# Kernel tuning notes

Hardware: AMD Instinct MI355X
Metric: run time of the kernel (lower is better)

The kernel has to match this reference:

```python
import jax, jax.numpy as jnp
import numpy as np
from jax import lax

NUM_TAGS = 9
HIDDEN = 768
BATCH = 64
SEQ = 512


def setup_inputs() -> dict:
    key = jax.random.key(0)
    ks = jax.random.split(key, 6)
    hidden = jax.random.normal(ks[0], (BATCH, SEQ, HIDDEN), dtype=jnp.float32)
    labels = jax.random.randint(ks[1], (BATCH, SEQ), 0, NUM_TAGS)  # all >= 0 -> full mask
    weight = jax.random.normal(ks[2], (NUM_TAGS, HIDDEN), dtype=jnp.float32) * 0.02
    bias = jnp.zeros((NUM_TAGS,), dtype=jnp.float32)
    start_transitions = jax.random.normal(ks[3], (NUM_TAGS,), dtype=jnp.float32) * 0.1
    end_transitions = jax.random.normal(ks[4], (NUM_TAGS,), dtype=jnp.float32) * 0.1
    transitions = jax.random.normal(ks[5], (NUM_TAGS, NUM_TAGS), dtype=jnp.float32) * 0.1
    return dict(hidden=hidden, labels=labels, weight=weight, bias=bias,
                start_transitions=start_transitions, end_transitions=end_transitions,
                transitions=transitions)


def _crf_log_likelihood(emissions, tags, mask, start_t, end_t, trans):
    """pytorch-crf log-likelihood, reduction='sum'.
    emissions [B,L,T] float, tags [B,L] int, mask [B,L] bool."""
    # --- numerator: score of the gold path ---
    tag0 = tags[:, 0]
    score0 = start_t[tag0] + jnp.take_along_axis(emissions[:, 0], tag0[:, None], axis=1)[:, 0]

    def num_step(carry, inp):
        score, prev = carry
        em, tg, m = inp  # em [B,T], tg [B], m [B]
        s = trans[prev, tg] + jnp.take_along_axis(em, tg[:, None], axis=1)[:, 0]
        score = score + jnp.where(m, s, jnp.zeros_like(s))
        prev = jnp.where(m, tg, prev)
        return (score, prev), None

    (num_score, last_tag), _ = lax.scan(
        num_step, (score0, tag0),
        (emissions[:, 1:].swapaxes(0, 1), tags[:, 1:].T, mask[:, 1:].T))
    numerator = num_score + end_t[last_tag]

    # --- denominator: forward algorithm (log-sum-exp recurrence) ---
    alpha0 = start_t[None, :] + emissions[:, 0]  # [B,T]

    def den_step(alpha, inp):
        em, m = inp  # em [B,T], m [B]
        nxt = jax.nn.logsumexp(alpha[:, :, None] + trans[None], axis=1) + em
        alpha = jnp.where(m[:, None], nxt, alpha)
        return alpha, None

    alpha, _ = lax.scan(den_step, alpha0,
                        (emissions[:, 1:].swapaxes(0, 1), mask[:, 1:].T))
    denominator = jax.nn.logsumexp(alpha + end_t[None, :], axis=1)

    return jnp.sum(numerator - denominator)


def _viterbi_decode(emissions, mask, start_t, end_t, trans):
    """Max-plus DP + backtrack. Returns padded [B,L] int32 best tag sequence."""
    B, L, T = emissions.shape
    score0 = start_t[None, :] + emissions[:, 0]  # [B,T]
    identity = jnp.arange(T, dtype=jnp.int32)[None, :]  # identity backpointer for masked steps

    def fwd_step(score, inp):
        em, m = inp  # em [B,T], m [B]
        br = score[:, :, None] + trans[None]  # [B,T_prev,T_cur]
        idx = jnp.argmax(br, axis=1).astype(jnp.int32)  # [B,T]
        nxt = jnp.max(br, axis=1) + em
        score = jnp.where(m[:, None], nxt, score)
        idx = jnp.where(m[:, None], idx, identity)
        return score, idx

    final, hist = lax.scan(fwd_step, score0,
                           (emissions[:, 1:].swapaxes(0, 1), mask[:, 1:].T))
    last_tag = jnp.argmax(final + end_t[None, :], axis=1).astype(jnp.int32)  # [B]

    def back_step(tag, idx):  # idx [B,T] backpointers for this position
        prev = jnp.take_along_axis(idx, tag[:, None], axis=1)[:, 0]
        return prev, tag

    first_tag, tags_rev = lax.scan(back_step, last_tag, hist, reverse=True)
    tags = jnp.concatenate([first_tag[None, :], tags_rev], axis=0).T  # [B,L]
    return tags * mask.astype(jnp.int32)


def reference(hidden, labels, weight, bias, start_transitions, end_transitions, transitions):
    mask_full = labels >= 0
    h = hidden[:, 1:-1, :]                       # drop [CLS]/[SEP] positions
    tags = labels[:, 1:-1] * mask_full[:, 1:-1]  # zero out padded labels
    mask = mask_full[:, 1:-1]
    # dropout is identity in eval mode
    emissions = jnp.einsum('blh,th->blt', h, weight) + bias  # [B,L,T]
    llh = _crf_log_likelihood(emissions, tags, mask,
                              start_transitions, end_transitions, transitions)
    tag_seqs = _viterbi_decode(emissions, mask,
                               start_transitions, end_transitions, transitions)
    return -llh, tag_seqs.astype(jnp.float32)
```

## Files before the change

### kernel.cpp

```cpp
#include <hip/hip_runtime.h>
#include <stdint.h>

#define NB 64
#define SEQL 512
#define L 510
#define T 9
#define H 768
#define EMS 12
#define LN2 0.6931471805599453f

__device__ __forceinline__ float rl(float v, int l) {
  return __uint_as_float(__builtin_amdgcn_readlane(__float_as_uint(v), l));
}

__global__ __launch_bounds__(256) void emis_kernel(
    const float* __restrict__ hidden, const float* __restrict__ weight,
    const float* __restrict__ bias, float* __restrict__ em,
    float* __restrict__ eem, float* __restrict__ out) {
  __shared__ float4 wl[T * 192];
  const float4* w4 = (const float4*)weight;
  for (int k = threadIdx.x; k < T * 192; k += 256) wl[k] = w4[k];
  if (blockIdx.x == 0 && threadIdx.x == 0) out[0] = 0.f;
  __syncthreads();
  const int lane = threadIdx.x & 63;
  const int wv = threadIdx.x >> 6;
  const int base = blockIdx.x * 64 + wv * 16;
#pragma unroll 1
  for (int pr = 0; pr < 8; ++pr) {
    const int r0 = base + pr * 2, r1 = r0 + 1;
    const int b0 = r0 / L, p0 = r0 - b0 * L;
    const int b1 = r1 / L, p1 = r1 - b1 * L;
    const float4* h0 = (const float4*)(hidden + ((size_t)(b0 * SEQL + p0 + 1)) * H);
    const float4* h1 = (const float4*)(hidden + ((size_t)(b1 * SEQL + p1 + 1)) * H);
    float4 ha[3], hb[3];
#pragma unroll
    for (int k = 0; k < 3; ++k) { ha[k] = h0[lane + 64 * k]; hb[k] = h1[lane + 64 * k]; }
    float a0[T], a1[T];
#pragma unroll
    for (int t = 0; t < T; ++t) { a0[t] = 0.f; a1[t] = 0.f; }
#pragma unroll
    for (int t = 0; t < T; ++t) {
#pragma unroll
      for (int k = 0; k < 3; ++k) {
        float4 w = wl[t * 192 + lane + 64 * k];
        a0[t] = fmaf(ha[k].x, w.x, fmaf(ha[k].y, w.y, fmaf(ha[k].z, w.z, fmaf(ha[k].w, w.w, a0[t]))));
        a1[t] = fmaf(hb[k].x, w.x, fmaf(hb[k].y, w.y, fmaf(hb[k].z, w.z, fmaf(hb[k].w, w.w, a1[t]))));
      }
    }
#pragma unroll
    for (int off = 32; off; off >>= 1) {
#pragma unroll
      for (int t = 0; t < T; ++t) {
        a0[t] += __shfl_xor(a0[t], off);
        a1[t] += __shfl_xor(a1[t], off);
      }
    }
    if (lane < 2) {
      const int rr = lane ? r1 : r0;
      float* eo = em + (size_t)rr * EMS;
      float* xo = eem + (size_t)rr * EMS;
#pragma unroll
      for (int t = 0; t < T; ++t) {
        float v = (lane ? a1[t] : a0[t]) + bias[t];
        eo[t] = v;
        xo[t] = __expf(v);
      }
    }
  }
}

__global__ __launch_bounds__(64) void chunk_kernel(
    const float* __restrict__ em, const float* __restrict__ eem,
    const float* __restrict__ trans, float* __restrict__ PdLn,
    float* __restrict__ Mv) {
  const int lane = threadIdx.x;
  const int m7 = lane / 9;
  const int i9 = lane - m7 * 9;
  const bool isden = blockIdx.x < 147;
  const int wid = isden ? blockIdx.x : blockIdx.x - 147;
  const int rtask = wid * 7 + (m7 < 7 ? m7 : 6);
  const bool act = (m7 < 7) && (rtask < 1024);
  const int task = act ? rtask : 0;
  const int b = task >> 4, s = task & 15;
  const int nt = (s == 15) ? 29 : 32;
  const int l0 = 32 * s + 1;

  if (isden) {
    float E[81];
#pragma unroll
    for (int k = 0; k < 81; ++k) E[k] = __expf(trans[k]);
    const float* ee = eem + ((size_t)(b * L + l0)) * EMS;
    float4 ea = *(const float4*)(ee);
    float4 eb = *(const float4*)(ee + 4);
    float e8 = ee[8];
    float ec[9] = {ea.x, ea.y, ea.z, ea.w, eb.x, eb.y, eb.z, eb.w, e8};
    float R[9];
#pragma unroll
    for (int j = 0; j < 9; ++j) R[j] = E[i9 * 9 + j] * ec[j];
    int iexp = 0;
    float4 na = *(const float4*)(ee + EMS);
    float4 nb = *(const float4*)(ee + EMS + 4);
    float n8 = ee[EMS + 8];
    for (int t = 1; t < nt; ++t) {
      float e0 = na.x, e1 = na.y, e2 = na.z, e3 = na.w;
      float e4 = nb.x, e5 = nb.y, e6 = nb.z, e7 = nb.w, e8c = n8;
      if (t < nt - 1) {
        na = *(const float4*)(ee + (size_t)(t + 1) * EMS);
        nb = *(const float4*)(ee + (size_t)(t + 1) * EMS + 4);
        n8 = ee[(size_t)(t + 1) * EMS + 8];
      }
      float Rn[9];
#pragma unroll
      for (int j = 0; j < 9; ++j) {
        float a = R[0] * E[0 * 9 + j];
#pragma unroll
        for (int k = 1; k < 9; ++k) a = fmaf(R[k], E[k * 9 + j], a);
        Rn[j] = a;
      }
      R[0] = Rn[0] * e0; R[1] = Rn[1] * e1; R[2] = Rn[2] * e2;
      R[3] = Rn[3] * e3; R[4] = Rn[4] * e4; R[5] = Rn[5] * e5;
      R[6] = Rn[6] * e6; R[7] = Rn[7] * e7; R[8] = Rn[8] * e8c;
      if ((t & 3) == 0) {
        float mx = R[0];
#pragma unroll
        for (int j = 1; j < 9; ++j) mx = fmaxf(mx, R[j]);
        int ex = (int)((__float_as_uint(mx) >> 23) & 0xff) - 127;
        iexp += ex;
        float sc = __uint_as_float((uint32_t)(127 - ex) << 23);
#pragma unroll
        for (int j = 0; j < 9; ++j) R[j] *= sc;
      }
    }
    if (act) {
      float ls = (float)iexp * LN2;
#pragma unroll
      for (int j = 0; j < 9; ++j)
        PdLn[(size_t)task * 81 + j * 9 + i9] = __logf(R[j]) + ls;
    }
  } else {
    float t_[81];
#pragma unroll
    for (int k = 0; k < 81; ++k) t_[k] = trans[k];
    const float* ep = em + ((size_t)(b * L + l0)) * EMS;
    float4 ea = *(const float4*)(ep);
    float4 eb = *(const float4*)(ep + 4);
    float e8 = ep[8];
    float ec[9] = {ea.x, ea.y, ea.z, ea.w, eb.x, eb.y, eb.z, eb.w, e8};
    float V[9];
#pragma unroll
    for (int j = 0; j < 9; ++j) V[j] = t_[i9 * 9 + j] + ec[j];
    float4 na = *(const float4*)(ep + EMS);
    float4 nb = *(const float4*)(ep + EMS + 4);
    float n8 = ep[EMS + 8];
    for (int t = 1; t < nt; ++t) {
      float e[9] = {na.x, na.y, na.z, na.w, nb.x, nb.y, nb.z, nb.w, n8};
      if (t < nt - 1) {
        na = *(const float4*)(ep + (size_t)(t + 1) * EMS);
        nb = *(const float4*)(ep + (size_t)(t + 1) * EMS + 4);
        n8 = ep[(size_t)(t + 1) * EMS + 8];
      }
      float Vn[9];
#pragma unroll
      for (int j = 0; j < 9; ++j) {
        float m = V[0] + t_[0 * 9 + j];
#pragma unroll
        for (int k = 1; k < 9; ++k) m = fmaxf(m, V[k] + t_[k * 9 + j]);
        Vn[j] = m + e[j];
      }
#pragma unroll
      for (int j = 0; j < 9; ++j) V[j] = Vn[j];
    }
    if (act) {
#pragma unroll
      for (int j = 0; j < 9; ++j)
        Mv[(size_t)task * 81 + j * 9 + i9] = V[j];
    }
  }
}

__global__ __launch_bounds__(64) void compose_kernel(
    const float* __restrict__ em, const int* __restrict__ labels,
    const float* __restrict__ PdLn, const float* __restrict__ Mv,
    const float* __restrict__ start_t, const float* __restrict__ end_t,
    const float* __restrict__ trans, unsigned char* __restrict__ chosen,
    float* __restrict__ out) {
  __shared__ float s_pd[16 * 81];
  __shared__ float s_mv[16 * 81];
  __shared__ float s_A[17 * 9];
  __shared__ float s_t[81];
  __shared__ int s_lab[L];
  const int b = blockIdx.x;
  const int lane = threadIdx.x;
  for (int k = lane; k < 16 * 81; k += 64) {
    s_pd[k] = PdLn[(size_t)b * 16 * 81 + k];
    s_mv[k] = Mv[(size_t)b * 16 * 81 + k];
  }
  for (int k = lane; k < 81; k += 64) s_t[k] = trans[k];
  for (int k = lane; k < L; k += 64) s_lab[k] = labels[b * SEQL + 1 + k];
  __syncthreads();

  const int jj = lane < 9 ? lane : 8;

  float part = 0.f;
  for (int l = lane; l < L; l += 64) {
    int tg = s_lab[l];
    float e = em[((size_t)(b * L + l)) * EMS + tg];
    if (l == 0) part += start_t[tg] + e;
    else part += s_t[s_lab[l - 1] * 9 + tg] + e;
    if (l == L - 1) part += end_t[tg];
  }
#pragma unroll
  for (int off = 32; off; off >>= 1) part += __shfl_xor(part, off);

  float D = start_t[jj] + em[(size_t)b * L * EMS + jj];
  for (int s = 0; s < 16; ++s) {
    const float* col = &s_pd[s * 81 + jj * 9];
    float v0 = rl(D, 0) + col[0], v1 = rl(D, 1) + col[1], v2 = rl(D, 2) + col[2];
    float v3 = rl(D, 3) + col[3], v4 = rl(D, 4) + col[4], v5 = rl(D, 5) + col[5];
    float v6 = rl(D, 6) + col[6], v7 = rl(D, 7) + col[7], v8 = rl(D, 8) + col[8];
    float mx = fmaxf(fmaxf(fmaxf(fmaxf(v0, v1), fmaxf(v2, v3)),
                           fmaxf(fmaxf(v4, v5), fmaxf(v6, v7))), v8);
    float sum = __expf(v0 - mx) + __expf(v1 - mx) + __expf(v2 - mx) +
                __expf(v3 - mx) + __expf(v4 - mx) + __expf(v5 - mx) +
                __expf(v6 - mx) + __expf(v7 - mx) + __expf(v8 - mx);
    D = mx + __logf(sum);
  }
  float fe = D + end_t[jj];
  float w0 = rl(fe, 0), w1 = rl(fe, 1), w2 = rl(fe, 2), w3 = rl(fe, 3);
  float w4 = rl(fe, 4), w5 = rl(fe, 5), w6 = rl(fe, 6), w7 = rl(fe, 7), w8 = rl(fe, 8);
  float mx = fmaxf(fmaxf(fmaxf(fmaxf(w0, w1), fmaxf(w2, w3)),
                         fmaxf(fmaxf(w4, w5), fmaxf(w6, w7))), w8);
  float den = mx + __logf(__expf(w0 - mx) + __expf(w1 - mx) + __expf(w2 - mx) +
                          __expf(w3 - mx) + __expf(w4 - mx) + __expf(w5 - mx) +
                          __expf(w6 - mx) + __expf(w7 - mx) + __expf(w8 - mx));
  if (lane == 0) atomicAdd(out, den - part);

  float A = start_t[jj] + em[(size_t)b * L * EMS + jj];
  if (lane < 9) s_A[lane] = A;
  for (int s = 0; s < 16; ++s) {
    const float* col = &s_mv[s * 81 + jj * 9];
    float u0 = rl(A, 0) + col[0], u1 = rl(A, 1) + col[1], u2 = rl(A, 2) + col[2];
    float u3 = rl(A, 3) + col[3], u4 = rl(A, 4) + col[4], u5 = rl(A, 5) + col[5];
    float u6 = rl(A, 6) + col[6], u7 = rl(A, 7) + col[7], u8 = rl(A, 8) + col[8];
    A = fmaxf(fmaxf(fmaxf(fmaxf(u0, u1), fmaxf(u2, u3)),
                    fmaxf(fmaxf(u4, u5), fmaxf(u6, u7))), u8);
    if (lane < 9) s_A[(s + 1) * 9 + lane] = A;
  }
  float fv = A + end_t[jj];
  int j = 0;
  {
    float bv = rl(fv, 0);
#pragma unroll
    for (int i = 1; i < 9; ++i) { float v = rl(fv, i); if (v > bv) { bv = v; j = i; } }
  }
  for (int s = 15; s >= 0; --s) {
    float val = s_A[s * 9 + jj] + s_mv[s * 81 + j * 9 + jj];
    int ii = 0;
    float bb = rl(val, 0);
#pragma unroll
    for (int i = 1; i < 9; ++i) { float v = rl(val, i); if (v > bb) { bb = v; ii = i; } }
    if (lane == 0) {
      chosen[(b * 16 + s) * 2] = (unsigned char)ii;
      chosen[(b * 16 + s) * 2 + 1] = (unsigned char)j;
    }
    j = ii;
  }
  if (lane == 0) out[1 + (size_t)b * L] = (float)j;
}

__global__ __launch_bounds__(64) void path_kernel(
    const float* __restrict__ em, const float* __restrict__ trans,
    const unsigned char* __restrict__ chosen, float* __restrict__ out) {
  __shared__ float s_t[81];
  __shared__ uint32_t s_bp[32][64][2];
  const int lane = threadIdx.x;
  for (int k = lane; k < 81; k += 64) s_t[k] = trans[k];
  __syncthreads();
  const int task = blockIdx.x * 64 + lane;
  const int b = task >> 4, s = task & 15;
  const int nt = (s == 15) ? 29 : 32;
  const int l0 = 32 * s + 1;
  const int i0 = chosen[task * 2];
  const int jF = chosen[task * 2 + 1];
  float t_[81];
#pragma unroll
  for (int k = 0; k < 81; ++k) t_[k] = trans[k];
  const float* ep = em + ((size_t)(b * L + l0)) * EMS;
  float a[9];
  {
    float4 ea = *(const float4*)(ep);
    float4 eb = *(const float4*)(ep + 4);
    float e8 = ep[8];
    float e[9] = {ea.x, ea.y, ea.z, ea.w, eb.x, eb.y, eb.z, eb.w, e8};
#pragma unroll
    for (int jx = 0; jx < 9; ++jx) a[jx] = s_t[i0 * 9 + jx] + e[jx];
  }
  for (int q = 1; q < nt; ++q) {
    float4 na = *(const float4*)(ep + (size_t)q * EMS);
    float4 nb = *(const float4*)(ep + (size_t)q * EMS + 4);
    float n8 = ep[(size_t)q * EMS + 8];
    float e[9] = {na.x, na.y, na.z, na.w, nb.x, nb.y, nb.z, nb.w, n8};
    uint32_t pk0 = 0, pk1 = 0;
    float an[9];
#pragma unroll
    for (int jx = 0; jx < 9; ++jx) {
      float best = a[0] + t_[0 * 9 + jx];
      int bi = 0;
#pragma unroll
      for (int k = 1; k < 9; ++k) {
        float v = a[k] + t_[k * 9 + jx];
        if (v > best) { best = v; bi = k; }
      }
      an[jx] = best + e[jx];
      if (jx < 8) pk0 |= ((uint32_t)bi) << (4 * jx);
      else pk1 = (uint32_t)bi;
    }
    s_bp[q][lane][0] = pk0;
    s_bp[q][lane][1] = pk1;
#pragma unroll
    for (int jx = 0; jx < 9; ++jx) a[jx] = an[jx];
  }
  int cur = jF;
  float* orow = out + 1 + (size_t)b * L + l0;
  for (int q = nt - 1; q >= 1; --q) {
    orow[q] = (float)cur;
    uint32_t w = s_bp[q][lane][cur >> 3];
    cur = (int)((w >> ((cur & 7) * 4)) & 15u);
  }
  orow[0] = (float)cur;
}

extern "C" void kernel_launch(void* const* d_in, const int* in_sizes, int n_in,
                              void* d_out, int out_size, void* d_ws, size_t ws_size,
                              hipStream_t stream) {
  const float* hidden  = (const float*)d_in[0];
  const int*   labels  = (const int*)d_in[1];
  const float* weight  = (const float*)d_in[2];
  const float* bias    = (const float*)d_in[3];
  const float* start_t = (const float*)d_in[4];
  const float* end_t   = (const float*)d_in[5];
  const float* trans   = (const float*)d_in[6];
  float* out = (float*)d_out;

  float* em   = (float*)d_ws;
  float* eem  = em + (size_t)NB * L * EMS;
  float* PdLn = eem + (size_t)NB * L * EMS;
  float* Mv   = PdLn + (size_t)1024 * 81;
  unsigned char* chosen = (unsigned char*)(Mv + (size_t)1024 * 81);

  emis_kernel<<<510, 256, 0, stream>>>(hidden, weight, bias, em, eem, out);
  chunk_kernel<<<294, 64, 0, stream>>>(em, eem, trans, PdLn, Mv);
  compose_kernel<<<NB, 64, 0, stream>>>(em, labels, PdLn, Mv, start_t, end_t,
                                        trans, chosen, out);
  path_kernel<<<16, 64, 0, stream>>>(em, trans, chosen, out);
}
```

Measured before the change: 223.5 us.

## Fuse emission and chunk kernels, and compose and path kernels via LDS

Merges the emission GEMV with the per-chunk forward/Viterbi recurrences, so each block computes 64 rows of one batch into shared memory and its four waves run the chunk scans from LDS. The separate eem buffer and its global round-trip go away. The compose and path-backtrace kernels are also merged: the per-batch emission row is staged in LDS and 16 lanes redo the chunk backtraces, which removes two launches and the chosen buffer. The cost is lower parallelism in the backtrace (16 blocks of 64 lanes become 64 blocks with 16 active lanes) and serial recurrences now sitting behind the GEMV in the same block.

```diff
diff --git a/kernel.cpp b/kernel.cpp
--- a/kernel.cpp
+++ b/kernel.cpp
@@ -13,25 +13,35 @@
   return __uint_as_float(__builtin_amdgcn_readlane(__float_as_uint(v), l));
 }
 
-__global__ __launch_bounds__(256) void emis_kernel(
+__global__ __launch_bounds__(256) void emis_chunk_kernel(
     const float* __restrict__ hidden, const float* __restrict__ weight,
-    const float* __restrict__ bias, float* __restrict__ em,
-    float* __restrict__ eem, float* __restrict__ out) {
+    const float* __restrict__ bias, const float* __restrict__ trans,
+    float* __restrict__ em, float* __restrict__ PdLn, float* __restrict__ Mv,
+    float* __restrict__ out) {
   __shared__ float4 wl[T * 192];
+  __shared__ __align__(16) float s_em[65][12];
+  __shared__ __align__(16) float s_ee[65][12];
   const float4* w4 = (const float4*)weight;
   for (int k = threadIdx.x; k < T * 192; k += 256) wl[k] = w4[k];
   if (blockIdx.x == 0 && threadIdx.x == 0) out[0] = 0.f;
   __syncthreads();
+  const int b = blockIdx.x >> 3;
+  const int p = blockIdx.x & 7;
+  const int row0 = p * 64;
   const int lane = threadIdx.x & 63;
   const int wv = threadIdx.x >> 6;
-  const int base = blockIdx.x * 64 + wv * 16;
+  const int npair = (wv == 0) ? 9 : 8;
 #pragma unroll 1
-  for (int pr = 0; pr < 8; ++pr) {
-    const int r0 = base + pr * 2, r1 = r0 + 1;
-    const int b0 = r0 / L, p0 = r0 - b0 * L;
-    const int b1 = r1 / L, p1 = r1 - b1 * L;
-    const float4* h0 = (const float4*)(hidden + ((size_t)(b0 * SEQL + p0 + 1)) * H);
-    const float4* h1 = (const float4*)(hidden + ((size_t)(b1 * SEQL + p1 + 1)) * H);
+  for (int pr = 0; pr < npair; ++pr) {
+    const int i0 = (pr < 8) ? (wv * 16 + pr * 2) : 64;
+    const int i1 = (pr < 8) ? (i0 + 1) : 64;
+    const int r0 = row0 + i0, r1 = row0 + i1;
+    const bool v0 = (r0 < L);
+    const bool v1 = (r1 < L) && (pr < 8);
+    const int c0 = v0 ? r0 : 0;
+    const int c1 = (r1 < L) ? r1 : 0;
+    const float4* h0 = (const float4*)(hidden + ((size_t)(b * SEQL + c0 + 1)) * H);
+    const float4* h1 = (const float4*)(hidden + ((size_t)(b * SEQL + c1 + 1)) * H);
     float4 ha[3], hb[3];
 #pragma unroll
     for (int k = 0; k < 3; ++k) { ha[k] = h0[lane + 64 * k]; hb[k] = h1[lane + 64 * k]; }
@@ -56,70 +66,51 @@
       }
     }
     if (lane < 2) {
-      const int rr = lane ? r1 : r0;
-      float* eo = em + (size_t)rr * EMS;
-      float* xo = eem + (size_t)rr * EMS;
-#pragma unroll
-      for (int t = 0; t < T; ++t) {
-        float v = (lane ? a1[t] : a0[t]) + bias[t];
-        eo[t] = v;
-        xo[t] = __expf(v);
-      }
-    }
-  }
-}
-
-__global__ __launch_bounds__(64) void chunk_kernel(
-    const float* __restrict__ em, const float* __restrict__ eem,
-    const float* __restrict__ trans, float* __restrict__ PdLn,
-    float* __restrict__ Mv) {
-  const int lane = threadIdx.x;
-  const int m7 = lane / 9;
-  const int i9 = lane - m7 * 9;
-  const bool isden = blockIdx.x < 147;
-  const int wid = isden ? blockIdx.x : blockIdx.x - 147;
-  const int rtask = wid * 7 + (m7 < 7 ? m7 : 6);
-  const bool act = (m7 < 7) && (rtask < 1024);
-  const int task = act ? rtask : 0;
-  const int b = task >> 4, s = task & 15;
-  const int nt = (s == 15) ? 29 : 32;
-  const int l0 = 32 * s + 1;
-
-  if (isden) {
+      const bool vv = lane ? v1 : v0;
+      const int ii = lane ? i1 : i0;
+      if (vv) {
+#pragma unroll
+        for (int t = 0; t < T; ++t) {
+          float v = (lane ? a1[t] : a0[t]) + bias[t];
+          s_em[ii][t] = v;
+          s_ee[ii][t] = __expf(v);
+        }
+      }
+    }
+  }
+  __syncthreads();
+  {
+    const int nf4 = (p == 7) ? 186 : 192;
+    if (threadIdx.x < nf4) {
+      float4* dst = (float4*)(em + ((size_t)(b * L + row0)) * EMS);
+      dst[threadIdx.x] = ((const float4*)s_em)[threadIdx.x];
+    }
+  }
+  const int cb = wv & 1;
+  const int sc_ = 2 * p + cb;
+  const int task = b * 16 + sc_;
+  const int nt = (sc_ == 15) ? 29 : 32;
+  const int base = 1 + 32 * cb;
+  const int i9 = (lane < 9) ? lane : 8;
+  if (wv < 2) {
     float E[81];
 #pragma unroll
     for (int k = 0; k < 81; ++k) E[k] = __expf(trans[k]);
-    const float* ee = eem + ((size_t)(b * L + l0)) * EMS;
-    float4 ea = *(const float4*)(ee);
-    float4 eb = *(const float4*)(ee + 4);
-    float e8 = ee[8];
-    float ec[9] = {ea.x, ea.y, ea.z, ea.w, eb.x, eb.y, eb.z, eb.w, e8};
     float R[9];
 #pragma unroll
-    for (int j = 0; j < 9; ++j) R[j] = E[i9 * 9 + j] * ec[j];
+    for (int j = 0; j < 9; ++j) R[j] = E[i9 * 9 + j] * s_ee[base][j];
     int iexp = 0;
-    float4 na = *(const float4*)(ee + EMS);
-    float4 nb = *(const float4*)(ee + EMS + 4);
-    float n8 = ee[EMS + 8];
     for (int t = 1; t < nt; ++t) {
-      float e0 = na.x, e1 = na.y, e2 = na.z, e3 = na.w;
-      float e4 = nb.x, e5 = nb.y, e6 = nb.z, e7 = nb.w, e8c = n8;
-      if (t < nt - 1) {
-        na = *(const float4*)(ee + (size_t)(t + 1) * EMS);
-        nb = *(const float4*)(ee + (size_t)(t + 1) * EMS + 4);
-        n8 = ee[(size_t)(t + 1) * EMS + 8];
-      }
       float Rn[9];
 #pragma unroll
       for (int j = 0; j < 9; ++j) {
-        float a = R[0] * E[0 * 9 + j];
+        float a = R[0] * E[j];
 #pragma unroll
         for (int k = 1; k < 9; ++k) a = fmaf(R[k], E[k * 9 + j], a);
         Rn[j] = a;
       }
-      R[0] = Rn[0] * e0; R[1] = Rn[1] * e1; R[2] = Rn[2] * e2;
-      R[3] = Rn[3] * e3; R[4] = Rn[4] * e4; R[5] = Rn[5] * e5;
-      R[6] = Rn[6] * e6; R[7] = Rn[7] * e7; R[8] = Rn[8] * e8c;
+#pragma unroll
+      for (int j = 0; j < 9; ++j) R[j] = Rn[j] * s_ee[base + t][j];
       if ((t & 3) == 0) {
         float mx = R[0];
 #pragma unroll
@@ -131,7 +122,7 @@
         for (int j = 0; j < 9; ++j) R[j] *= sc;
       }
     }
-    if (act) {
+    if (lane < 9) {
       float ls = (float)iexp * LN2;
 #pragma unroll
       for (int j = 0; j < 9; ++j)
@@ -141,36 +132,22 @@
     float t_[81];
 #pragma unroll
     for (int k = 0; k < 81; ++k) t_[k] = trans[k];
-    const float* ep = em + ((size_t)(b * L + l0)) * EMS;
-    float4 ea = *(const float4*)(ep);
-    float4 eb = *(const float4*)(ep + 4);
-    float e8 = ep[8];
-    float ec[9] = {ea.x, ea.y, ea.z, ea.w, eb.x, eb.y, eb.z, eb.w, e8};
     float V[9];
 #pragma unroll
-    for (int j = 0; j < 9; ++j) V[j] = t_[i9 * 9 + j] + ec[j];
-    float4 na = *(const float4*)(ep + EMS);
-    float4 nb = *(const float4*)(ep + EMS + 4);
-    float n8 = ep[EMS + 8];
+    for (int j = 0; j < 9; ++j) V[j] = t_[i9 * 9 + j] + s_em[base][j];
     for (int t = 1; t < nt; ++t) {
-      float e[9] = {na.x, na.y, na.z, na.w, nb.x, nb.y, nb.z, nb.w, n8};
-      if (t < nt - 1) {
-        na = *(const float4*)(ep + (size_t)(t + 1) * EMS);
-        nb = *(const float4*)(ep + (size_t)(t + 1) * EMS + 4);
-        n8 = ep[(size_t)(t + 1) * EMS + 8];
-      }
       float Vn[9];
 #pragma unroll
       for (int j = 0; j < 9; ++j) {
         float m = V[0] + t_[0 * 9 + j];
 #pragma unroll
         for (int k = 1; k < 9; ++k) m = fmaxf(m, V[k] + t_[k * 9 + j]);
-        Vn[j] = m + e[j];
+        Vn[j] = m + s_em[base + t][j];
       }
 #pragma unroll
       for (int j = 0; j < 9; ++j) V[j] = Vn[j];
     }
-    if (act) {
+    if (lane < 9) {
 #pragma unroll
       for (int j = 0; j < 9; ++j)
         Mv[(size_t)task * 81 + j * 9 + i9] = V[j];
@@ -178,19 +155,27 @@
   }
 }
 
-__global__ __launch_bounds__(64) void compose_kernel(
+#define EADDR(l) ((l) * 12 + ((l) >> 5) * 4)
+__global__ __launch_bounds__(64) void compose_path_kernel(
     const float* __restrict__ em, const int* __restrict__ labels,
     const float* __restrict__ PdLn, const float* __restrict__ Mv,
     const float* __restrict__ start_t, const float* __restrict__ end_t,
-    const float* __restrict__ trans, unsigned char* __restrict__ chosen,
-    float* __restrict__ out) {
+    const float* __restrict__ trans, float* __restrict__ out) {
   __shared__ float s_pd[16 * 81];
   __shared__ float s_mv[16 * 81];
   __shared__ float s_A[17 * 9];
   __shared__ float s_t[81];
   __shared__ int s_lab[L];
+  __shared__ __align__(16) float s_e[510 * 12 + 64];
+  __shared__ uint32_t s_bp[32][16][2];
+  __shared__ int s_ch[16][2];
   const int b = blockIdx.x;
   const int lane = threadIdx.x;
+  const float4* eg = (const float4*)(em + (size_t)b * L * EMS);
+  for (int k = lane; k < 1530; k += 64) {
+    const int l = k / 3, part = k - l * 3;
+    *(float4*)&s_e[(size_t)EADDR(l) + part * 4] = eg[k];
+  }
   for (int k = lane; k < 16 * 81; k += 64) {
     s_pd[k] = PdLn[(size_t)b * 16 * 81 + k];
     s_mv[k] = Mv[(size_t)b * 16 * 81 + k];
@@ -201,20 +186,20 @@
 
   const int jj = lane < 9 ? lane : 8;
 
-  float part = 0.f;
+  float part_ = 0.f;
   for (int l = lane; l < L; l += 64) {
     int tg = s_lab[l];
-    float e = em[((size_t)(b * L + l)) * EMS + tg];
-    if (l == 0) part += start_t[tg] + e;
-    else part += s_t[s_lab[l - 1] * 9 + tg] + e;
-    if (l == L - 1) part += end_t[tg];
-  }
-#pragma unroll
-  for (int off = 32; off; off >>= 1) part += __shfl_xor(part, off);
-
-  float D = start_t[jj] + em[(size_t)b * L * EMS + jj];
-  for (int s = 0; s < 16; ++s) {
-    const float* col = &s_pd[s * 81 + jj * 9];
+    float e = s_e[EADDR(l) + tg];
+    if (l == 0) part_ += start_t[tg] + e;
+    else part_ += s_t[s_lab[l - 1] * 9 + tg] + e;
+    if (l == L - 1) part_ += end_t[tg];
+  }
+#pragma unroll
+  for (int off = 32; off; off >>= 1) part_ += __shfl_xor(part_, off);
+
+  float D = start_t[jj] + s_e[jj];
+  for (int u = 0; u < 16; ++u) {
+    const float* col = &s_pd[u * 81 + jj * 9];
     float v0 = rl(D, 0) + col[0], v1 = rl(D, 1) + col[1], v2 = rl(D, 2) + col[2];
     float v3 = rl(D, 3) + col[3], v4 = rl(D, 4) + col[4], v5 = rl(D, 5) + col[5];
     float v6 = rl(D, 6) + col[6], v7 = rl(D, 7) + col[7], v8 = rl(D, 8) + col[8];
@@ -233,18 +218,18 @@
   float den = mx + __logf(__expf(w0 - mx) + __expf(w1 - mx) + __expf(w2 - mx) +
                           __expf(w3 - mx) + __expf(w4 - mx) + __expf(w5 - mx) +
                           __expf(w6 - mx) + __expf(w7 - mx) + __expf(w8 - mx));
-  if (lane == 0) atomicAdd(out, den - part);
-
-  float A = start_t[jj] + em[(size_t)b * L * EMS + jj];
+  if (lane == 0) atomicAdd(out, den - part_);
+
+  float A = start_t[jj] + s_e[jj];
   if (lane < 9) s_A[lane] = A;
-  for (int s = 0; s < 16; ++s) {
-    const float* col = &s_mv[s * 81 + jj * 9];
+  for (int u = 0; u < 16; ++u) {
+    const float* col = &s_mv[u * 81 + jj * 9];
     float u0 = rl(A, 0) + col[0], u1 = rl(A, 1) + col[1], u2 = rl(A, 2) + col[2];
     float u3 = rl(A, 3) + col[3], u4 = rl(A, 4) + col[4], u5 = rl(A, 5) + col[5];
     float u6 = rl(A, 6) + col[6], u7 = rl(A, 7) + col[7], u8 = rl(A, 8) + col[8];
     A = fmaxf(fmaxf(fmaxf(fmaxf(u0, u1), fmaxf(u2, u3)),
                     fmaxf(fmaxf(u4, u5), fmaxf(u6, u7))), u8);
-    if (lane < 9) s_A[(s + 1) * 9 + lane] = A;
+    if (lane < 9) s_A[(u + 1) * 9 + lane] = A;
   }
   float fv = A + end_t[jj];
   int j = 0;
@@ -253,81 +238,64 @@
 #pragma unroll
     for (int i = 1; i < 9; ++i) { float v = rl(fv, i); if (v > bv) { bv = v; j = i; } }
   }
-  for (int s = 15; s >= 0; --s) {
-    float val = s_A[s * 9 + jj] + s_mv[s * 81 + j * 9 + jj];
+  for (int u = 15; u >= 0; --u) {
+    float val = s_A[u * 9 + jj] + s_mv[u * 81 + j * 9 + jj];
     int ii = 0;
     float bb = rl(val, 0);
 #pragma unroll
     for (int i = 1; i < 9; ++i) { float v = rl(val, i); if (v > bb) { bb = v; ii = i; } }
-    if (lane == 0) {
-      chosen[(b * 16 + s) * 2] = (unsigned char)ii;
-      chosen[(b * 16 + s) * 2 + 1] = (unsigned char)j;
-    }
+    if (lane == 0) { s_ch[u][0] = ii; s_ch[u][1] = j; }
     j = ii;
   }
   if (lane == 0) out[1 + (size_t)b * L] = (float)j;
-}
-
-__global__ __launch_bounds__(64) void path_kernel(
-    const float* __restrict__ em, const float* __restrict__ trans,
-    const unsigned char* __restrict__ chosen, float* __restrict__ out) {
-  __shared__ float s_t[81];
-  __shared__ uint32_t s_bp[32][64][2];
-  const int lane = threadIdx.x;
-  for (int k = lane; k < 81; k += 64) s_t[k] = trans[k];
   __syncthreads();
-  const int task = blockIdx.x * 64 + lane;
-  const int b = task >> 4, s = task & 15;
-  const int nt = (s == 15) ? 29 : 32;
-  const int l0 = 32 * s + 1;
-  const int i0 = chosen[task * 2];
-  const int jF = chosen[task * 2 + 1];
-  float t_[81];
-#pragma unroll
-  for (int k = 0; k < 81; ++k) t_[k] = trans[k];
-  const float* ep = em + ((size_t)(b * L + l0)) * EMS;
-  float a[9];
-  {
-    float4 ea = *(const float4*)(ep);
-    float4 eb = *(const float4*)(ep + 4);
-    float e8 = ep[8];
-    float e[9] = {ea.x, ea.y, ea.z, ea.w, eb.x, eb.y, eb.z, eb.w, e8};
-#pragma unroll
-    for (int jx = 0; jx < 9; ++jx) a[jx] = s_t[i0 * 9 + jx] + e[jx];
-  }
-  for (int q = 1; q < nt; ++q) {
-    float4 na = *(const float4*)(ep + (size_t)q * EMS);
-    float4 nb = *(const float4*)(ep + (size_t)q * EMS + 4);
-    float n8 = ep[(size_t)q * EMS + 8];
-    float e[9] = {na.x, na.y, na.z, na.w, nb.x, nb.y, nb.z, nb.w, n8};
-    uint32_t pk0 = 0, pk1 = 0;
-    float an[9];
-#pragma unroll
-    for (int jx = 0; jx < 9; ++jx) {
-      float best = a[0] + t_[0 * 9 + jx];
-      int bi = 0;
-#pragma unroll
-      for (int k = 1; k < 9; ++k) {
-        float v = a[k] + t_[k * 9 + jx];
-        if (v > best) { best = v; bi = k; }
-      }
-      an[jx] = best + e[jx];
-      if (jx < 8) pk0 |= ((uint32_t)bi) << (4 * jx);
-      else pk1 = (uint32_t)bi;
-    }
-    s_bp[q][lane][0] = pk0;
-    s_bp[q][lane][1] = pk1;
-#pragma unroll
-    for (int jx = 0; jx < 9; ++jx) a[jx] = an[jx];
-  }
-  int cur = jF;
-  float* orow = out + 1 + (size_t)b * L + l0;
-  for (int q = nt - 1; q >= 1; --q) {
-    orow[q] = (float)cur;
-    uint32_t w = s_bp[q][lane][cur >> 3];
-    cur = (int)((w >> ((cur & 7) * 4)) & 15u);
-  }
-  orow[0] = (float)cur;
+
+  if (lane < 16) {
+    const int sch = lane;
+    const int nt = (sch == 15) ? 29 : 32;
+    const int lb = 32 * sch + 1;
+    const int i0 = s_ch[sch][0];
+    const int jF = s_ch[sch][1];
+    float t_[81];
+#pragma unroll
+    for (int k = 0; k < 81; ++k) t_[k] = trans[k];
+    float a[9];
+    {
+      const int ea = EADDR(lb);
+#pragma unroll
+      for (int jx = 0; jx < 9; ++jx) a[jx] = s_t[i0 * 9 + jx] + s_e[ea + jx];
+    }
+    for (int q = 1; q < nt; ++q) {
+      const int ea = EADDR(lb + q);
+      uint32_t pk0 = 0, pk1 = 0;
+      float an[9];
+#pragma unroll
+      for (int jx = 0; jx < 9; ++jx) {
+        float best = a[0] + t_[0 * 9 + jx];
+        int bi = 0;
+#pragma unroll
+        for (int k = 1; k < 9; ++k) {
+          float v = a[k] + t_[k * 9 + jx];
+          if (v > best) { best = v; bi = k; }
+        }
+        an[jx] = best + s_e[ea + jx];
+        if (jx < 8) pk0 |= ((uint32_t)bi) << (4 * jx);
+        else pk1 = (uint32_t)bi;
+      }
+      s_bp[q][sch][0] = pk0;
+      s_bp[q][sch][1] = pk1;
+#pragma unroll
+      for (int jx = 0; jx < 9; ++jx) a[jx] = an[jx];
+    }
+    int cur = jF;
+    float* orow = out + 1 + (size_t)b * L + lb;
+    for (int q = nt - 1; q >= 1; --q) {
+      orow[q] = (float)cur;
+      uint32_t w = s_bp[q][sch][cur >> 3];
+      cur = (int)((w >> ((cur & 7) * 4)) & 15u);
+    }
+    orow[0] = (float)cur;
+  }
 }
 
 extern "C" void kernel_launch(void* const* d_in, const int* in_sizes, int n_in,
@@ -343,14 +311,11 @@
   float* out = (float*)d_out;
 
   float* em   = (float*)d_ws;
-  float* eem  = em + (size_t)NB * L * EMS;
-  float* PdLn = eem + (size_t)NB * L * EMS;
+  float* PdLn = em + (size_t)NB * L * EMS;
   float* Mv   = PdLn + (size_t)1024 * 81;
-  unsigned char* chosen = (unsigned char*)(Mv + (size_t)1024 * 81);
-
-  emis_kernel<<<510, 256, 0, stream>>>(hidden, weight, bias, em, eem, out);
-  chunk_kernel<<<294, 64, 0, stream>>>(em, eem, trans, PdLn, Mv);
-  compose_kernel<<<NB, 64, 0, stream>>>(em, labels, PdLn, Mv, start_t, end_t,
-                                        trans, chosen, out);
-  path_kernel<<<16, 64, 0, stream>>>(em, trans, chosen, out);
+
+  emis_chunk_kernel<<<512, 256, 0, stream>>>(hidden, weight, bias, trans,
+                                             em, PdLn, Mv, out);
+  compose_path_kernel<<<NB, 64, 0, stream>>>(em, labels, PdLn, Mv,
+                                             start_t, end_t, trans, out);
 }
```

Result: slower. 242.1 us (+8.3%).
